# Kernel tuning notes

Hardware: AMD Instinct MI355X
Metric: run time of the kernel (lower is better)

The kernel has to match this reference:

```python
import jax, jax.numpy as jnp
import numpy as np

B, S, E, H = 2, 2048, 1024, 16
D = E // H  # head_dim = 64
NEG = -1e9


def setup_inputs() -> dict:
    key = jax.random.key(0)
    ks = jax.random.split(key, 12)
    def xavier(k, shape):
        fan_in, fan_out = shape[1], shape[0]
        lim = jnp.sqrt(6.0 / (fan_in + fan_out))
        return jax.random.uniform(k, shape, jnp.float32, -lim, lim)
    inp = {
        'Q_input': jax.random.normal(ks[0], (B, S, E), jnp.float32),
        'K_input': jax.random.normal(ks[1], (B, S, E), jnp.float32),
        'V_input': jax.random.normal(ks[2], (B, S, E), jnp.float32),
        'causal_mask': jnp.where(jnp.tril(jnp.ones((S, S), bool)), 0.0, NEG).astype(jnp.float32),
        'padding_mask': jnp.zeros((B, S), bool),
        'W_q': xavier(ks[3], (E, E)), 'b_q': jnp.zeros((E,), jnp.float32),
        'W_k': xavier(ks[4], (E, E)), 'b_k': jnp.zeros((E,), jnp.float32),
        'W_v': xavier(ks[5], (E, E)), 'b_v': jnp.zeros((E,), jnp.float32),
        'W_o': xavier(ks[6], (E, E)), 'b_o': jnp.zeros((E,), jnp.float32),
    }
    return inp


def reference(Q_input, K_input, V_input, causal_mask, padding_mask,
              W_q, b_q, W_k, b_k, W_v, b_v, W_o, b_o):
    b = Q_input.shape[0]
    # linear proj (torch convention: x @ W.T + b), split into heads -> [B,H,S,D]
    def proj(x, W, bias):
        y = x @ W.T + bias
        return y.reshape(b, -1, H, D).transpose(0, 2, 1, 3)
    Q = proj(Q_input, W_q, b_q)
    K = proj(K_input, W_k, b_k)
    V = proj(V_input, W_v, b_v)
    scale = 1.0 / jnp.sqrt(jnp.float32(D))
    scores = jnp.einsum('bhqd,bhkd->bhqk', Q, K) * scale  # [B,H,Sq,Sk]
    scores = jnp.where(padding_mask[:, None, None, :], NEG, scores)
    scores = scores + causal_mask  # broadcasts [Sq,Sk]
    attn = jax.nn.softmax(scores, axis=-1)
    ctx = jnp.einsum('bhqk,bhkd->bhqd', attn, V)
    ctx = ctx.transpose(0, 2, 1, 3).reshape(b, -1, E)
    return ctx @ W_o.T + b_o
```

## Files before the change

kernel.cpp:

```cpp
#include <hip/hip_runtime.h>
#include <hip/hip_bf16.h>

#define B_ 2
#define S_ 2048
#define E_ 1024
#define H_ 16
#define D_ 64

typedef __bf16 bf16x8 __attribute__((ext_vector_type(8)));
typedef __bf16 bf16x4 __attribute__((ext_vector_type(4)));
typedef float f32x4 __attribute__((ext_vector_type(4)));

#define MFMA16(a, b, c) __builtin_amdgcn_mfma_f32_16x16x32_bf16(a, b, c, 0, 0, 0)

__device__ __forceinline__ void cp16(const void* g, void* l) {
  __builtin_amdgcn_global_load_lds((const __attribute__((address_space(1))) void*)g,
                                   (__attribute__((address_space(3))) void*)l, 16, 0, 0);
}

__device__ __forceinline__ unsigned pack2(float a, float b) {
  unsigned short ua = __builtin_bit_cast(unsigned short, (__bf16)a);
  unsigned short ub = __builtin_bit_cast(unsigned short, (__bf16)b);
  return (unsigned)ua | ((unsigned)ub << 16);
}

__global__ __launch_bounds__(256) void cast_weights(
    const float* __restrict__ w0, const float* __restrict__ w1,
    const float* __restrict__ w2, const float* __restrict__ w3,
    __bf16* __restrict__ out)
{
  const float* srcs[4] = {w0, w1, w2, w3};
  const float* src = srcs[blockIdx.y];
  __bf16* dst = out + (size_t)blockIdx.y * E_ * E_;
  int i = (blockIdx.x * 256 + threadIdx.x) * 8;
  f32x4 a = *(const f32x4*)(src + i);
  f32x4 b = *(const f32x4*)(src + i + 4);
  bf16x8 o;
#pragma unroll
  for (int j = 0; j < 4; ++j) { o[j] = (__bf16)a[j]; o[j + 4] = (__bf16)b[j]; }
  *(bf16x8*)(dst + i) = o;
}

__global__ __launch_bounds__(256) void gemm_qkv(
    const float* __restrict__ Xq, const float* __restrict__ Xk,
    const float* __restrict__ Xv, const __bf16* __restrict__ Wc,
    const float* __restrict__ bq, const float* __restrict__ bk,
    const float* __restrict__ bv, __bf16* __restrict__ Proj)
{
  __shared__ __bf16 As[128 * 40];
  __shared__ __bf16 Bs[128 * 32];

  const int tid  = threadIdx.x;
  const int wave = tid >> 6, lane = tid & 63;
  const int l15  = lane & 15, quad = lane >> 4;
  const int wr = wave >> 1, wc = wave & 1;
  const int m0 = blockIdx.x * 128;
  const int wid = blockIdx.y >> 3;
  const int n0 = (blockIdx.y & 7) * 128;

  const float* X    = wid == 0 ? Xq : (wid == 1 ? Xk : Xv);
  const float* bias = wid == 0 ? bq : (wid == 1 ? bk : bv);
  const __bf16* W   = Wc + (size_t)wid * E_ * E_;
  __bf16* Out       = Proj + (size_t)wid * B_ * S_ * E_;

  f32x4 acc[4][4];
#pragma unroll
  for (int i = 0; i < 4; ++i)
#pragma unroll
    for (int j = 0; j < 4; ++j) acc[i][j] = (f32x4){0, 0, 0, 0};

  for (int k0 = 0; k0 < E_; k0 += 32) {
#pragma unroll
    for (int i = 0; i < 2; ++i) {
      int c = i * 256 + tid;
      int row = c >> 2, cg = c & 3;
      cp16(W + (size_t)(n0 + row) * E_ + k0 + cg * 8,
           (char*)Bs + i * 4096 + wave * 1024);
    }
#pragma unroll
    for (int i = 0; i < 2; ++i) {
      int c = i * 256 + tid;
      int row = c >> 2, cg = c & 3;
      f32x4 x0 = *(const f32x4*)(X + (size_t)(m0 + row) * E_ + k0 + cg * 8);
      f32x4 x1 = *(const f32x4*)(X + (size_t)(m0 + row) * E_ + k0 + cg * 8 + 4);
      bf16x8 v;
#pragma unroll
      for (int j = 0; j < 4; ++j) { v[j] = (__bf16)x0[j]; v[j + 4] = (__bf16)x1[j]; }
      *(bf16x8*)&As[row * 40 + cg * 8] = v;
    }
    __syncthreads();

    bf16x8 af[4], bfr[4];
#pragma unroll
    for (int ms = 0; ms < 4; ++ms) {
      int row = wr * 64 + ms * 16 + l15;
      af[ms] = *(const bf16x8*)&As[row * 40 + quad * 8];
    }
#pragma unroll
    for (int ns = 0; ns < 4; ++ns) {
      int row = wc * 64 + ns * 16 + l15;
      bfr[ns] = *(const bf16x8*)((const char*)Bs + row * 64 + quad * 16);
    }
#pragma unroll
    for (int ms = 0; ms < 4; ++ms)
#pragma unroll
      for (int ns = 0; ns < 4; ++ns)
        acc[ms][ns] = MFMA16(af[ms], bfr[ns], acc[ms][ns]);
    __syncthreads();
  }

#pragma unroll
  for (int ns = 0; ns < 4; ++ns) {
    int n = n0 + wc * 64 + ns * 16 + l15;
    float bv_ = bias[n];
#pragma unroll
    for (int ms = 0; ms < 4; ++ms)
#pragma unroll
      for (int r = 0; r < 4; ++r) {
        int m = m0 + wr * 64 + ms * 16 + quad * 4 + r;
        Out[(size_t)m * E_ + n] = (__bf16)(acc[ms][ns][r] + bv_);
      }
  }
}

__global__ __launch_bounds__(256) void gemm_out(
    const __bf16* __restrict__ X, const __bf16* __restrict__ W,
    const float* __restrict__ bias, float* __restrict__ out)
{
  __shared__ __bf16 As[64 * 32];
  __shared__ __bf16 Bs[128 * 32];

  const int tid  = threadIdx.x;
  const int wave = tid >> 6, lane = tid & 63;
  const int l15  = lane & 15, quad = lane >> 4;
  const int wr = wave >> 1, wc = wave & 1;
  const int m0 = blockIdx.x * 64;
  const int n0 = blockIdx.y * 128;

  f32x4 acc[2][4];
#pragma unroll
  for (int i = 0; i < 2; ++i)
#pragma unroll
    for (int j = 0; j < 4; ++j) acc[i][j] = (f32x4){0, 0, 0, 0};

  for (int k0 = 0; k0 < E_; k0 += 32) {
    {
      int row = tid >> 2, cg = tid & 3;
      cp16(X + (size_t)(m0 + row) * E_ + k0 + cg * 8,
           (char*)As + wave * 1024);
    }
#pragma unroll
    for (int i = 0; i < 2; ++i) {
      int c = i * 256 + tid;
      int row = c >> 2, cg = c & 3;
      cp16(W + (size_t)(n0 + row) * E_ + k0 + cg * 8,
           (char*)Bs + i * 4096 + wave * 1024);
    }
    __syncthreads();

    bf16x8 af[2], bfr[4];
#pragma unroll
    for (int ms = 0; ms < 2; ++ms) {
      int row = wr * 32 + ms * 16 + l15;
      af[ms] = *(const bf16x8*)((const char*)As + row * 64 + quad * 16);
    }
#pragma unroll
    for (int ns = 0; ns < 4; ++ns) {
      int row = wc * 64 + ns * 16 + l15;
      bfr[ns] = *(const bf16x8*)((const char*)Bs + row * 64 + quad * 16);
    }
#pragma unroll
    for (int ms = 0; ms < 2; ++ms)
#pragma unroll
      for (int ns = 0; ns < 4; ++ns)
        acc[ms][ns] = MFMA16(af[ms], bfr[ns], acc[ms][ns]);
    __syncthreads();
  }

#pragma unroll
  for (int ns = 0; ns < 4; ++ns) {
    int n = n0 + wc * 64 + ns * 16 + l15;
    float bv_ = bias[n];
#pragma unroll
    for (int ms = 0; ms < 2; ++ms)
#pragma unroll
      for (int r = 0; r < 4; ++r) {
        int m = m0 + wr * 32 + ms * 16 + quad * 4 + r;
        out[(size_t)m * E_ + n] = acc[ms][ns][r] + bv_;
      }
  }
}

__global__ __launch_bounds__(64) void transpose_v(
    const __bf16* __restrict__ Vp, __bf16* __restrict__ Vt)
{
  const int lane = threadIdx.x;
  const int b = blockIdx.y >> 4;
  const int h = blockIdx.y & 15;
  const int s0 = blockIdx.x * 64 + (lane & 7) * 8;
  const int d0 = (lane >> 3) * 8;

  bf16x8 in[8];
#pragma unroll
  for (int j = 0; j < 8; ++j)
    in[j] = *(const bf16x8*)&Vp[(((size_t)b * S_ + s0 + j) * H_ + h) * D_ + d0];
#pragma unroll
  for (int i = 0; i < 8; ++i) {
    bf16x8 t;
#pragma unroll
    for (int j = 0; j < 8; ++j) t[j] = in[j][i];
    *(bf16x8*)&Vt[(((size_t)b * H_ + h) * D_ + d0 + i) * S_ + s0] = t;
  }
}

__global__ __launch_bounds__(256) void attn_fwd(
    const __bf16* __restrict__ Qp, const __bf16* __restrict__ Kp,
    const __bf16* __restrict__ Vt, __bf16* __restrict__ Ctx)
{
  const int tid  = threadIdx.x;
  const int wave = tid >> 6;
  const int lane = tid & 63;
  const int l15  = lane & 15;
  const int quad = lane >> 4;
  const int t  = (int)gridDim.x - 1 - (int)blockIdx.x;
  const int q0 = t * 64;
  const int b  = blockIdx.y >> 4;
  const int h  = blockIdx.y & 15;
  const int wq0 = q0 + wave * 16;

  __shared__ __bf16 Ksh[2][64 * 64];
  __shared__ __bf16 Vsh[2][64 * 64];

  const __bf16* Khb = Kp + (size_t)b * S_ * E_ + h * 64;
  const __bf16* Vhb = Vt + ((size_t)b * H_ + h) * D_ * S_;

  bf16x8 qa[2];
#pragma unroll
  for (int kk = 0; kk < 2; ++kk) {
    bf16x8 q = *(const bf16x8*)&Qp[(size_t)(b * S_ + wq0 + l15) * E_ + h * 64 + kk * 32 + quad * 8];
#pragma unroll
    for (int j = 0; j < 8; ++j) q[j] = (__bf16)((float)q[j] * 0.125f);
    qa[kk] = q;
  }

  f32x4 o[4];
  float rs = 0.f;
#pragma unroll
  for (int ds = 0; ds < 4; ++ds) o[ds] = (f32x4){0, 0, 0, 0};

  const int nch = t + 1;

  auto stage = [&](int c, int bi) {
    const int kb0 = c * 64;
#pragma unroll
    for (int i = 0; i < 2; ++i) {
      int cc = i * 256 + tid;
      int key = cc >> 3, p = cc & 7;
      int pg = p ^ (key & 7);
      cp16(Khb + (size_t)(kb0 + key) * E_ + pg * 8,
           (char*)&Ksh[bi][0] + i * 4096 + wave * 1024);
    }
#pragma unroll
    for (int i = 0; i < 2; ++i) {
      int cc = i * 256 + tid;
      int d = cc >> 3, kp = cc & 7;
      int kpg = kp ^ (d & 7);
      cp16(Vhb + (size_t)d * S_ + kb0 + kpg * 8,
           (char*)&Vsh[bi][0] + i * 4096 + wave * 1024);
    }
  };

  stage(0, 0);

  const int hb = quad >> 1;
  const int s0l = (2 * (quad & 1)) * 16 + l15;
  const int s1l = s0l + 16;

  int cur = 0;
  for (int c = 0; c < nch; ++c) {
    if (c + 1 < nch) {
      stage(c + 1, cur ^ 1);
      asm volatile("s_waitcnt vmcnt(4)" ::: "memory");
    } else {
      asm volatile("s_waitcnt vmcnt(0)" ::: "memory");
    }
    __builtin_amdgcn_s_barrier();

    const int kb0 = c * 64;

    f32x4 sc[4];
    __builtin_amdgcn_s_setprio(1);
#pragma unroll
    for (int ks = 0; ks < 4; ++ks) {
      const char* Kpan = (const char*)&Ksh[cur][0];
      int row = ks * 16 + l15;
      bf16x8 kf0 = *(const bf16x8*)(Kpan + row * 128 + (((quad)     ^ (l15 & 7)) * 16));
      bf16x8 kf1 = *(const bf16x8*)(Kpan + row * 128 + (((4 + quad) ^ (l15 & 7)) * 16));
      f32x4 s = {0, 0, 0, 0};
      s = MFMA16(kf0, qa[0], s);
      s = MFMA16(kf1, qa[1], s);
      sc[ks] = s;
    }
    __builtin_amdgcn_s_setprio(0);

    unsigned pw[4][2];
    const bool msk = (kb0 + 63 > wq0);
    if (msk) {
#pragma unroll
      for (int ks = 0; ks < 4; ++ks) {
        float p[4];
#pragma unroll
        for (int r = 0; r < 4; ++r) {
          float e = __expf(sc[ks][r]);
          if (kb0 + ks * 16 + quad * 4 + r > wq0 + l15) e = 0.f;
          rs += e;
          p[r] = e;
        }
        pw[ks][0] = pack2(p[0], p[1]);
        pw[ks][1] = pack2(p[2], p[3]);
      }
    } else {
#pragma unroll
      for (int ks = 0; ks < 4; ++ks) {
        float p[4];
#pragma unroll
        for (int r = 0; r < 4; ++r) {
          float e = __expf(sc[ks][r]);
          rs += e;
          p[r] = e;
        }
        pw[ks][0] = pack2(p[0], p[1]);
        pw[ks][1] = pack2(p[2], p[3]);
      }
    }

    bf16x8 pf[2];
#pragma unroll
    for (int kk = 0; kk < 2; ++kk) {
      unsigned w[4];
#pragma unroll
      for (int wi = 0; wi < 4; ++wi) {
        int src = (wi & 2) ? s1l : s0l;
        unsigned g0 = __shfl(pw[2 * kk + 0][wi & 1], src, 64);
        unsigned g1 = __shfl(pw[2 * kk + 1][wi & 1], src, 64);
        w[wi] = hb ? g1 : g0;
      }
      union { unsigned u[4]; bf16x8 v; } cvt;
      cvt.u[0] = w[0]; cvt.u[1] = w[1]; cvt.u[2] = w[2]; cvt.u[3] = w[3];
      pf[kk] = cvt.v;
    }

    __builtin_amdgcn_s_setprio(1);
#pragma unroll
    for (int ds = 0; ds < 4; ++ds) {
      int row = ds * 16 + l15;
#pragma unroll
      for (int kk = 0; kk < 2; ++kk) {
        const char* Vpan = (const char*)&Vsh[cur][0];
        bf16x8 vf = *(const bf16x8*)(Vpan + row * 128 +
                                     (((kk * 4 + quad) ^ (l15 & 7)) * 16));
        o[ds] = MFMA16(pf[kk], vf, o[ds]);
      }
    }
    __builtin_amdgcn_s_setprio(0);

    asm volatile("" ::: "memory");
    __builtin_amdgcn_s_barrier();
    asm volatile("" ::: "memory");
    cur ^= 1;
  }

  float s = rs;
  s += __shfl_xor(s, 16, 64);
  s += __shfl_xor(s, 32, 64);
  float inv = 1.f / s;

#pragma unroll
  for (int r = 0; r < 4; ++r) {
    float invr = __shfl(inv, quad * 4 + r, 64);
    size_t base = (size_t)(b * S_ + wq0 + quad * 4 + r) * E_ + h * 64;
#pragma unroll
    for (int ds = 0; ds < 4; ++ds)
      Ctx[base + ds * 16 + l15] = (__bf16)(o[ds][r] * invr);
  }
}

extern "C" void kernel_launch(void* const* d_in, const int* in_sizes, int n_in,
                              void* d_out, int out_size, void* d_ws, size_t ws_size,
                              hipStream_t stream)
{
  const float* Qin = (const float*)d_in[0];
  const float* Kin = (const float*)d_in[1];
  const float* Vin = (const float*)d_in[2];
  const float* Wq = (const float*)d_in[5];
  const float* bq = (const float*)d_in[6];
  const float* Wk = (const float*)d_in[7];
  const float* bk = (const float*)d_in[8];
  const float* Wv = (const float*)d_in[9];
  const float* bv = (const float*)d_in[10];
  const float* Wo = (const float*)d_in[11];
  const float* bo = (const float*)d_in[12];

  __bf16* ws = (__bf16*)d_ws;
  const size_t WSZ = (size_t)E_ * E_;
  const size_t T   = (size_t)B_ * S_ * E_;
  __bf16* Wc   = ws;
  __bf16* Proj = ws + 4 * WSZ;
  __bf16* Vt   = ws + 4 * WSZ + 3 * T;
  __bf16* Ctx  = ws + 4 * WSZ + 4 * T;

  cast_weights<<<dim3(512, 4), 256, 0, stream>>>(Wq, Wk, Wv, Wo, Wc);
  gemm_qkv<<<dim3(32, 24), 256, 0, stream>>>(Qin, Kin, Vin, Wc, bq, bk, bv, Proj);
  transpose_v<<<dim3(S_ / 64, B_ * H_), 64, 0, stream>>>(Proj + 2 * T, Vt);
  attn_fwd<<<dim3(S_ / 64, B_ * H_), 256, 0, stream>>>(Proj, Proj + T, Vt, Ctx);
  gemm_out<<<dim3(64, 8), 256, 0, stream>>>(Ctx, Wc + 3 * WSZ, bo, (float*)d_out);
}
```

Before: 270.5 us.

## Pre-cast activations to bf16, use async LDS loads in QKV GEMM, widen attention tiles

The QKV GEMM's per-tile fp32-to-bf16 conversion is replaced by one cast kernel that converts weights and all three inputs to bf16 in workspace. The GEMM then loads the A tile with direct global-to-LDS copies, dropping the padded layout. The attention kernel now handles 128 query rows per block, each wave owning two 16-row fragments that share each staged K/V chunk. It also uses a diagonal block-to-tile mapping for causal load balance and sets occupancy via launch bounds. The trade-offs are an extra fp32-to-bf16 pass with more workspace traffic, more registers per wave in attention, and half as many attention blocks.

```diff
diff --git a/kernel.cpp b/kernel.cpp
--- a/kernel.cpp
+++ b/kernel.cpp
@@ -24,15 +24,21 @@
   return (unsigned)ua | ((unsigned)ub << 16);
 }
 
-__global__ __launch_bounds__(256) void cast_weights(
+__global__ __launch_bounds__(256) void cast_all(
     const float* __restrict__ w0, const float* __restrict__ w1,
     const float* __restrict__ w2, const float* __restrict__ w3,
-    __bf16* __restrict__ out)
-{
-  const float* srcs[4] = {w0, w1, w2, w3};
-  const float* src = srcs[blockIdx.y];
-  __bf16* dst = out + (size_t)blockIdx.y * E_ * E_;
-  int i = (blockIdx.x * 256 + threadIdx.x) * 8;
+    const float* __restrict__ x0, const float* __restrict__ x1,
+    const float* __restrict__ x2,
+    __bf16* __restrict__ dW, __bf16* __restrict__ dX)
+{
+  const float* srcs[7] = {w0, w1, w2, w3, x0, x1, x2};
+  const int y = blockIdx.y;
+  const bool isW = y < 4;
+  const size_t n = isW ? (size_t)E_ * E_ : (size_t)B_ * S_ * E_;
+  size_t i = ((size_t)blockIdx.x * 256 + threadIdx.x) * 8;
+  if (i >= n) return;
+  const float* src = srcs[y];
+  __bf16* dst = isW ? dW + (size_t)y * E_ * E_ : dX + (size_t)(y - 4) * B_ * S_ * E_;
   f32x4 a = *(const f32x4*)(src + i);
   f32x4 b = *(const f32x4*)(src + i + 4);
   bf16x8 o;
@@ -42,12 +48,11 @@
 }
 
 __global__ __launch_bounds__(256) void gemm_qkv(
-    const float* __restrict__ Xq, const float* __restrict__ Xk,
-    const float* __restrict__ Xv, const __bf16* __restrict__ Wc,
+    const __bf16* __restrict__ Xb, const __bf16* __restrict__ Wc,
     const float* __restrict__ bq, const float* __restrict__ bk,
     const float* __restrict__ bv, __bf16* __restrict__ Proj)
 {
-  __shared__ __bf16 As[128 * 40];
+  __shared__ __bf16 As[128 * 32];
   __shared__ __bf16 Bs[128 * 32];
 
   const int tid  = threadIdx.x;
@@ -58,7 +63,7 @@
   const int wid = blockIdx.y >> 3;
   const int n0 = (blockIdx.y & 7) * 128;
 
-  const float* X    = wid == 0 ? Xq : (wid == 1 ? Xk : Xv);
+  const __bf16* X   = Xb + (size_t)wid * B_ * S_ * E_;
   const float* bias = wid == 0 ? bq : (wid == 1 ? bk : bv);
   const __bf16* W   = Wc + (size_t)wid * E_ * E_;
   __bf16* Out       = Proj + (size_t)wid * B_ * S_ * E_;
@@ -70,6 +75,13 @@
     for (int j = 0; j < 4; ++j) acc[i][j] = (f32x4){0, 0, 0, 0};
 
   for (int k0 = 0; k0 < E_; k0 += 32) {
+#pragma unroll
+    for (int i = 0; i < 2; ++i) {
+      int c = i * 256 + tid;
+      int row = c >> 2, cg = c & 3;
+      cp16(X + (size_t)(m0 + row) * E_ + k0 + cg * 8,
+           (char*)As + i * 4096 + wave * 1024);
+    }
 #pragma unroll
     for (int i = 0; i < 2; ++i) {
       int c = i * 256 + tid;
@@ -77,24 +89,13 @@
       cp16(W + (size_t)(n0 + row) * E_ + k0 + cg * 8,
            (char*)Bs + i * 4096 + wave * 1024);
     }
-#pragma unroll
-    for (int i = 0; i < 2; ++i) {
-      int c = i * 256 + tid;
-      int row = c >> 2, cg = c & 3;
-      f32x4 x0 = *(const f32x4*)(X + (size_t)(m0 + row) * E_ + k0 + cg * 8);
-      f32x4 x1 = *(const f32x4*)(X + (size_t)(m0 + row) * E_ + k0 + cg * 8 + 4);
-      bf16x8 v;
-#pragma unroll
-      for (int j = 0; j < 4; ++j) { v[j] = (__bf16)x0[j]; v[j + 4] = (__bf16)x1[j]; }
-      *(bf16x8*)&As[row * 40 + cg * 8] = v;
-    }
     __syncthreads();
 
     bf16x8 af[4], bfr[4];
 #pragma unroll
     for (int ms = 0; ms < 4; ++ms) {
       int row = wr * 64 + ms * 16 + l15;
-      af[ms] = *(const bf16x8*)&As[row * 40 + quad * 8];
+      af[ms] = *(const bf16x8*)((const char*)As + row * 64 + quad * 16);
     }
 #pragma unroll
     for (int ns = 0; ns < 4; ++ns) {
@@ -213,7 +214,7 @@
   }
 }
 
-__global__ __launch_bounds__(256) void attn_fwd(
+__global__ __launch_bounds__(256, 4) void attn_fwd(
     const __bf16* __restrict__ Qp, const __bf16* __restrict__ Kp,
     const __bf16* __restrict__ Vt, __bf16* __restrict__ Ctx)
 {
@@ -222,11 +223,13 @@
   const int lane = tid & 63;
   const int l15  = lane & 15;
   const int quad = lane >> 4;
-  const int t  = (int)gridDim.x - 1 - (int)blockIdx.x;
-  const int q0 = t * 64;
-  const int b  = blockIdx.y >> 4;
-  const int h  = blockIdx.y & 15;
-  const int wq0 = q0 + wave * 16;
+  const int x = blockIdx.x;
+  const int y = blockIdx.y;
+  const int t = (x + y + ((y >> 4) << 2)) & 15;
+  const int q0 = t * 128;
+  const int b  = y >> 4;
+  const int h  = y & 15;
+  const int wq0 = q0 + wave * 32;
 
   __shared__ __bf16 Ksh[2][64 * 64];
   __shared__ __bf16 Vsh[2][64 * 64];
@@ -234,21 +237,26 @@
   const __bf16* Khb = Kp + (size_t)b * S_ * E_ + h * 64;
   const __bf16* Vhb = Vt + ((size_t)b * H_ + h) * D_ * S_;
 
-  bf16x8 qa[2];
-#pragma unroll
-  for (int kk = 0; kk < 2; ++kk) {
-    bf16x8 q = *(const bf16x8*)&Qp[(size_t)(b * S_ + wq0 + l15) * E_ + h * 64 + kk * 32 + quad * 8];
-#pragma unroll
-    for (int j = 0; j < 8; ++j) q[j] = (__bf16)((float)q[j] * 0.125f);
-    qa[kk] = q;
-  }
-
-  f32x4 o[4];
-  float rs = 0.f;
-#pragma unroll
-  for (int ds = 0; ds < 4; ++ds) o[ds] = (f32x4){0, 0, 0, 0};
-
-  const int nch = t + 1;
+  bf16x8 qa[2][2];
+#pragma unroll
+  for (int f = 0; f < 2; ++f)
+#pragma unroll
+    for (int kk = 0; kk < 2; ++kk) {
+      bf16x8 q = *(const bf16x8*)&Qp[(size_t)(b * S_ + wq0 + f * 16 + l15) * E_ +
+                                     h * 64 + kk * 32 + quad * 8];
+#pragma unroll
+      for (int j = 0; j < 8; ++j) q[j] = (__bf16)((float)q[j] * 0.125f);
+      qa[f][kk] = q;
+    }
+
+  f32x4 o[2][4];
+  float rs[2] = {0.f, 0.f};
+#pragma unroll
+  for (int f = 0; f < 2; ++f)
+#pragma unroll
+    for (int ds = 0; ds < 4; ++ds) o[f][ds] = (f32x4){0, 0, 0, 0};
+
+  const int nch = 2 * t + 2;
 
   auto stage = [&](int c, int bi) {
     const int kb0 = c * 64;
@@ -287,82 +295,92 @@
     __builtin_amdgcn_s_barrier();
 
     const int kb0 = c * 64;
-
-    f32x4 sc[4];
-    __builtin_amdgcn_s_setprio(1);
-#pragma unroll
-    for (int ks = 0; ks < 4; ++ks) {
-      const char* Kpan = (const char*)&Ksh[cur][0];
-      int row = ks * 16 + l15;
-      bf16x8 kf0 = *(const bf16x8*)(Kpan + row * 128 + (((quad)     ^ (l15 & 7)) * 16));
-      bf16x8 kf1 = *(const bf16x8*)(Kpan + row * 128 + (((4 + quad) ^ (l15 & 7)) * 16));
-      f32x4 s = {0, 0, 0, 0};
-      s = MFMA16(kf0, qa[0], s);
-      s = MFMA16(kf1, qa[1], s);
-      sc[ks] = s;
-    }
-    __builtin_amdgcn_s_setprio(0);
-
-    unsigned pw[4][2];
-    const bool msk = (kb0 + 63 > wq0);
-    if (msk) {
-#pragma unroll
-      for (int ks = 0; ks < 4; ++ks) {
-        float p[4];
-#pragma unroll
-        for (int r = 0; r < 4; ++r) {
-          float e = __expf(sc[ks][r]);
-          if (kb0 + ks * 16 + quad * 4 + r > wq0 + l15) e = 0.f;
-          rs += e;
-          p[r] = e;
+    const bool act0 = (kb0 <= wq0 + 15);
+    if (kb0 <= wq0 + 31) {
+      bf16x8 pfB[2][2];
+
+#pragma unroll
+      for (int f = 0; f < 2; ++f) {
+        const int wqf = wq0 + f * 16;
+        if (kb0 > wqf + 15) continue;
+
+        f32x4 sc[4];
+        __builtin_amdgcn_s_setprio(1);
+#pragma unroll
+        for (int ks = 0; ks < 4; ++ks) {
+          const char* Kpan = (const char*)&Ksh[cur][0];
+          int row = ks * 16 + l15;
+          bf16x8 kf0 = *(const bf16x8*)(Kpan + row * 128 + (((quad)     ^ (l15 & 7)) * 16));
+          bf16x8 kf1 = *(const bf16x8*)(Kpan + row * 128 + (((4 + quad) ^ (l15 & 7)) * 16));
+          f32x4 s = {0, 0, 0, 0};
+          s = MFMA16(kf0, qa[f][0], s);
+          s = MFMA16(kf1, qa[f][1], s);
+          sc[ks] = s;
         }
-        pw[ks][0] = pack2(p[0], p[1]);
-        pw[ks][1] = pack2(p[2], p[3]);
+        __builtin_amdgcn_s_setprio(0);
+
+        unsigned pw[4][2];
+        const bool msk = (kb0 + 63 > wqf);
+        if (msk) {
+#pragma unroll
+          for (int ks = 0; ks < 4; ++ks) {
+            float p[4];
+#pragma unroll
+            for (int r = 0; r < 4; ++r) {
+              float e = __expf(sc[ks][r]);
+              if (kb0 + ks * 16 + quad * 4 + r > wqf + l15) e = 0.f;
+              rs[f] += e;
+              p[r] = e;
+            }
+            pw[ks][0] = pack2(p[0], p[1]);
+            pw[ks][1] = pack2(p[2], p[3]);
+          }
+        } else {
+#pragma unroll
+          for (int ks = 0; ks < 4; ++ks) {
+            float p[4];
+#pragma unroll
+            for (int r = 0; r < 4; ++r) {
+              float e = __expf(sc[ks][r]);
+              rs[f] += e;
+              p[r] = e;
+            }
+            pw[ks][0] = pack2(p[0], p[1]);
+            pw[ks][1] = pack2(p[2], p[3]);
+          }
+        }
+
+#pragma unroll
+        for (int kk = 0; kk < 2; ++kk) {
+          unsigned w[4];
+#pragma unroll
+          for (int wi = 0; wi < 4; ++wi) {
+            int src = (wi & 2) ? s1l : s0l;
+            unsigned g0 = __shfl(pw[2 * kk + 0][wi & 1], src, 64);
+            unsigned g1 = __shfl(pw[2 * kk + 1][wi & 1], src, 64);
+            w[wi] = hb ? g1 : g0;
+          }
+          union { unsigned u[4]; bf16x8 v; } cvt;
+          cvt.u[0] = w[0]; cvt.u[1] = w[1]; cvt.u[2] = w[2]; cvt.u[3] = w[3];
+          pfB[f][kk] = cvt.v;
+        }
       }
-    } else {
-#pragma unroll
-      for (int ks = 0; ks < 4; ++ks) {
-        float p[4];
-#pragma unroll
-        for (int r = 0; r < 4; ++r) {
-          float e = __expf(sc[ks][r]);
-          rs += e;
-          p[r] = e;
+
+      __builtin_amdgcn_s_setprio(1);
+#pragma unroll
+      for (int ds = 0; ds < 4; ++ds) {
+        int row = ds * 16 + l15;
+#pragma unroll
+        for (int kk = 0; kk < 2; ++kk) {
+          const char* Vpan = (const char*)&Vsh[cur][0];
+          bf16x8 vf = *(const bf16x8*)(Vpan + row * 128 +
+                                       (((kk * 4 + quad) ^ (l15 & 7)) * 16));
+          if (act0) o[0][ds] = MFMA16(pfB[0][kk], vf, o[0][ds]);
+          o[1][ds] = MFMA16(pfB[1][kk], vf, o[1][ds]);
         }
-        pw[ks][0] = pack2(p[0], p[1]);
-        pw[ks][1] = pack2(p[2], p[3]);
       }
-    }
-
-    bf16x8 pf[2];
-#pragma unroll
-    for (int kk = 0; kk < 2; ++kk) {
-      unsigned w[4];
-#pragma unroll
-      for (int wi = 0; wi < 4; ++wi) {
-        int src = (wi & 2) ? s1l : s0l;
-        unsigned g0 = __shfl(pw[2 * kk + 0][wi & 1], src, 64);
-        unsigned g1 = __shfl(pw[2 * kk + 1][wi & 1], src, 64);
-        w[wi] = hb ? g1 : g0;
-      }
-      union { unsigned u[4]; bf16x8 v; } cvt;
-      cvt.u[0] = w[0]; cvt.u[1] = w[1]; cvt.u[2] = w[2]; cvt.u[3] = w[3];
-      pf[kk] = cvt.v;
-    }
-
-    __builtin_amdgcn_s_setprio(1);
-#pragma unroll
-    for (int ds = 0; ds < 4; ++ds) {
-      int row = ds * 16 + l15;
-#pragma unroll
-      for (int kk = 0; kk < 2; ++kk) {
-        const char* Vpan = (const char*)&Vsh[cur][0];
-        bf16x8 vf = *(const bf16x8*)(Vpan + row * 128 +
-                                     (((kk * 4 + quad) ^ (l15 & 7)) * 16));
-        o[ds] = MFMA16(pf[kk], vf, o[ds]);
-      }
-    }
-    __builtin_amdgcn_s_setprio(0);
+      __builtin_amdgcn_s_setprio(0);
+    }
 
     asm volatile("" ::: "memory");
     __builtin_amdgcn_s_barrier();
@@ -370,18 +388,21 @@
     cur ^= 1;
   }
 
-  float s = rs;
-  s += __shfl_xor(s, 16, 64);
-  s += __shfl_xor(s, 32, 64);
-  float inv = 1.f / s;
-
-#pragma unroll
-  for (int r = 0; r < 4; ++r) {
-    float invr = __shfl(inv, quad * 4 + r, 64);
-    size_t base = (size_t)(b * S_ + wq0 + quad * 4 + r) * E_ + h * 64;
-#pragma unroll
-    for (int ds = 0; ds < 4; ++ds)
-      Ctx[base + ds * 16 + l15] = (__bf16)(o[ds][r] * invr);
+#pragma unroll
+  for (int f = 0; f < 2; ++f) {
+    float s = rs[f];
+    s += __shfl_xor(s, 16, 64);
+    s += __shfl_xor(s, 32, 64);
+    float inv = 1.f / s;
+
+#pragma unroll
+    for (int r = 0; r < 4; ++r) {
+      float invr = __shfl(inv, quad * 4 + r, 64);
+      size_t base = (size_t)(b * S_ + wq0 + f * 16 + quad * 4 + r) * E_ + h * 64;
+#pragma unroll
+      for (int ds = 0; ds < 4; ++ds)
+        Ctx[base + ds * 16 + l15] = (__bf16)(o[f][ds][r] * invr);
+    }
   }
 }
 
@@ -408,10 +429,11 @@
   __bf16* Proj = ws + 4 * WSZ;
   __bf16* Vt   = ws + 4 * WSZ + 3 * T;
   __bf16* Ctx  = ws + 4 * WSZ + 4 * T;
-
-  cast_weights<<<dim3(512, 4), 256, 0, stream>>>(Wq, Wk, Wv, Wo, Wc);
-  gemm_qkv<<<dim3(32, 24), 256, 0, stream>>>(Qin, Kin, Vin, Wc, bq, bk, bv, Proj);
+  __bf16* Xbf  = ws + 4 * WSZ + 5 * T;
+
+  cast_all<<<dim3(2048, 7), 256, 0, stream>>>(Wq, Wk, Wv, Wo, Qin, Kin, Vin, Wc, Xbf);
+  gemm_qkv<<<dim3(32, 24), 256, 0, stream>>>(Xbf, Wc, bq, bk, bv, Proj);
   transpose_v<<<dim3(S_ / 64, B_ * H_), 64, 0, stream>>>(Proj + 2 * T, Vt);
-  attn_fwd<<<dim3(S_ / 64, B_ * H_), 256, 0, stream>>>(Proj, Proj + T, Vt, Ctx);
+  attn_fwd<<<dim3(S_ / 128, B_ * H_), 256, 0, stream>>>(Proj, Proj + T, Vt, Ctx);
   gemm_out<<<dim3(64, 8), 256, 0, stream>>>(Ctx, Wc + 3 * WSZ, bo, (float*)d_out);
 }
```

Result: faster. 252.4 us (-6.7%).

## Pre-cast inputs to bf16, double-buffer GEMMs, pair causal attention tiles, use exp2

Applied to the files above, without the earlier changes.

Activations are now cast to bf16 in a separate pass, which lets the QKV GEMM load them with async global-to-LDS copies. Both GEMMs switch to double-buffered LDS with waitcnt-based prefetch and raised MFMA priority. Attention blocks each handle two query tiles (t and 31-t) to even out causal work, and apply the softmax scale as log2(e)/8 so they can use exp2f. The extra cast pass writes and then rereads a full bf16 copy of the inputs, and halving the attention grid lowers the number of concurrent blocks.

```diff
diff --git a/kernel.cpp b/kernel.cpp
--- a/kernel.cpp
+++ b/kernel.cpp
@@ -24,15 +24,21 @@
   return (unsigned)ua | ((unsigned)ub << 16);
 }
 
-__global__ __launch_bounds__(256) void cast_weights(
+__global__ __launch_bounds__(256) void cast_all(
     const float* __restrict__ w0, const float* __restrict__ w1,
     const float* __restrict__ w2, const float* __restrict__ w3,
-    __bf16* __restrict__ out)
-{
-  const float* srcs[4] = {w0, w1, w2, w3};
-  const float* src = srcs[blockIdx.y];
-  __bf16* dst = out + (size_t)blockIdx.y * E_ * E_;
-  int i = (blockIdx.x * 256 + threadIdx.x) * 8;
+    const float* __restrict__ x0, const float* __restrict__ x1,
+    const float* __restrict__ x2,
+    __bf16* __restrict__ dW, __bf16* __restrict__ dX)
+{
+  const float* srcs[7] = {w0, w1, w2, w3, x0, x1, x2};
+  const int y = blockIdx.y;
+  const bool isW = y < 4;
+  const size_t n = isW ? (size_t)E_ * E_ : (size_t)B_ * S_ * E_;
+  size_t i = ((size_t)blockIdx.x * 256 + threadIdx.x) * 8;
+  if (i >= n) return;
+  const float* src = srcs[y];
+  __bf16* dst = isW ? dW + (size_t)y * E_ * E_ : dX + (size_t)(y - 4) * B_ * S_ * E_;
   f32x4 a = *(const f32x4*)(src + i);
   f32x4 b = *(const f32x4*)(src + i + 4);
   bf16x8 o;
@@ -42,13 +48,12 @@
 }
 
 __global__ __launch_bounds__(256) void gemm_qkv(
-    const float* __restrict__ Xq, const float* __restrict__ Xk,
-    const float* __restrict__ Xv, const __bf16* __restrict__ Wc,
+    const __bf16* __restrict__ Xb, const __bf16* __restrict__ Wc,
     const float* __restrict__ bq, const float* __restrict__ bk,
     const float* __restrict__ bv, __bf16* __restrict__ Proj)
 {
-  __shared__ __bf16 As[128 * 40];
-  __shared__ __bf16 Bs[128 * 32];
+  __shared__ __bf16 As[2][128 * 32];
+  __shared__ __bf16 Bs[2][128 * 32];
 
   const int tid  = threadIdx.x;
   const int wave = tid >> 6, lane = tid & 63;
@@ -58,55 +63,68 @@
   const int wid = blockIdx.y >> 3;
   const int n0 = (blockIdx.y & 7) * 128;
 
-  const float* X    = wid == 0 ? Xq : (wid == 1 ? Xk : Xv);
+  const __bf16* X   = Xb + (size_t)wid * B_ * S_ * E_;
   const float* bias = wid == 0 ? bq : (wid == 1 ? bk : bv);
   const __bf16* W   = Wc + (size_t)wid * E_ * E_;
   __bf16* Out       = Proj + (size_t)wid * B_ * S_ * E_;
 
-  f32x4 acc[4][4];
-#pragma unroll
-  for (int i = 0; i < 4; ++i)
-#pragma unroll
-    for (int j = 0; j < 4; ++j) acc[i][j] = (f32x4){0, 0, 0, 0};
-
-  for (int k0 = 0; k0 < E_; k0 += 32) {
+  auto stage = [&](int k0, int bi) {
+#pragma unroll
+    for (int i = 0; i < 2; ++i) {
+      int c = i * 256 + tid;
+      int row = c >> 2, cg = c & 3;
+      cp16(X + (size_t)(m0 + row) * E_ + k0 + cg * 8,
+           (char*)&As[bi][0] + i * 4096 + wave * 1024);
+    }
 #pragma unroll
     for (int i = 0; i < 2; ++i) {
       int c = i * 256 + tid;
       int row = c >> 2, cg = c & 3;
       cp16(W + (size_t)(n0 + row) * E_ + k0 + cg * 8,
-           (char*)Bs + i * 4096 + wave * 1024);
-    }
-#pragma unroll
-    for (int i = 0; i < 2; ++i) {
-      int c = i * 256 + tid;
-      int row = c >> 2, cg = c & 3;
-      f32x4 x0 = *(const f32x4*)(X + (size_t)(m0 + row) * E_ + k0 + cg * 8);
-      f32x4 x1 = *(const f32x4*)(X + (size_t)(m0 + row) * E_ + k0 + cg * 8 + 4);
-      bf16x8 v;
-#pragma unroll
-      for (int j = 0; j < 4; ++j) { v[j] = (__bf16)x0[j]; v[j + 4] = (__bf16)x1[j]; }
-      *(bf16x8*)&As[row * 40 + cg * 8] = v;
-    }
-    __syncthreads();
+           (char*)&Bs[bi][0] + i * 4096 + wave * 1024);
+    }
+  };
+
+  f32x4 acc[4][4];
+#pragma unroll
+  for (int i = 0; i < 4; ++i)
+#pragma unroll
+    for (int j = 0; j < 4; ++j) acc[i][j] = (f32x4){0, 0, 0, 0};
+
+  stage(0, 0);
+  int cur = 0;
+  for (int k0 = 0; k0 < E_; k0 += 32) {
+    if (k0 + 32 < E_) {
+      stage(k0 + 32, cur ^ 1);
+      asm volatile("s_waitcnt vmcnt(4)" ::: "memory");
+    } else {
+      asm volatile("s_waitcnt vmcnt(0)" ::: "memory");
+    }
+    __builtin_amdgcn_s_barrier();
 
     bf16x8 af[4], bfr[4];
 #pragma unroll
     for (int ms = 0; ms < 4; ++ms) {
       int row = wr * 64 + ms * 16 + l15;
-      af[ms] = *(const bf16x8*)&As[row * 40 + quad * 8];
+      af[ms] = *(const bf16x8*)((const char*)&As[cur][0] + row * 64 + quad * 16);
     }
 #pragma unroll
     for (int ns = 0; ns < 4; ++ns) {
       int row = wc * 64 + ns * 16 + l15;
-      bfr[ns] = *(const bf16x8*)((const char*)Bs + row * 64 + quad * 16);
-    }
+      bfr[ns] = *(const bf16x8*)((const char*)&Bs[cur][0] + row * 64 + quad * 16);
+    }
+    __builtin_amdgcn_s_setprio(1);
 #pragma unroll
     for (int ms = 0; ms < 4; ++ms)
 #pragma unroll
       for (int ns = 0; ns < 4; ++ns)
         acc[ms][ns] = MFMA16(af[ms], bfr[ns], acc[ms][ns]);
-    __syncthreads();
+    __builtin_amdgcn_s_setprio(0);
+
+    asm volatile("" ::: "memory");
+    __builtin_amdgcn_s_barrier();
+    asm volatile("" ::: "memory");
+    cur ^= 1;
   }
 
 #pragma unroll
@@ -127,8 +145,8 @@
     const __bf16* __restrict__ X, const __bf16* __restrict__ W,
     const float* __restrict__ bias, float* __restrict__ out)
 {
-  __shared__ __bf16 As[64 * 32];
-  __shared__ __bf16 Bs[128 * 32];
+  __shared__ __bf16 As[2][64 * 32];
+  __shared__ __bf16 Bs[2][128 * 32];
 
   const int tid  = threadIdx.x;
   const int wave = tid >> 6, lane = tid & 63;
@@ -137,44 +155,61 @@
   const int m0 = blockIdx.x * 64;
   const int n0 = blockIdx.y * 128;
 
-  f32x4 acc[2][4];
-#pragma unroll
-  for (int i = 0; i < 2; ++i)
-#pragma unroll
-    for (int j = 0; j < 4; ++j) acc[i][j] = (f32x4){0, 0, 0, 0};
-
-  for (int k0 = 0; k0 < E_; k0 += 32) {
+  auto stage = [&](int k0, int bi) {
     {
       int row = tid >> 2, cg = tid & 3;
       cp16(X + (size_t)(m0 + row) * E_ + k0 + cg * 8,
-           (char*)As + wave * 1024);
+           (char*)&As[bi][0] + wave * 1024);
     }
 #pragma unroll
     for (int i = 0; i < 2; ++i) {
       int c = i * 256 + tid;
       int row = c >> 2, cg = c & 3;
       cp16(W + (size_t)(n0 + row) * E_ + k0 + cg * 8,
-           (char*)Bs + i * 4096 + wave * 1024);
-    }
-    __syncthreads();
+           (char*)&Bs[bi][0] + i * 4096 + wave * 1024);
+    }
+  };
+
+  f32x4 acc[2][4];
+#pragma unroll
+  for (int i = 0; i < 2; ++i)
+#pragma unroll
+    for (int j = 0; j < 4; ++j) acc[i][j] = (f32x4){0, 0, 0, 0};
+
+  stage(0, 0);
+  int cur = 0;
+  for (int k0 = 0; k0 < E_; k0 += 32) {
+    if (k0 + 32 < E_) {
+      stage(k0 + 32, cur ^ 1);
+      asm volatile("s_waitcnt vmcnt(3)" ::: "memory");
+    } else {
+      asm volatile("s_waitcnt vmcnt(0)" ::: "memory");
+    }
+    __builtin_amdgcn_s_barrier();
 
     bf16x8 af[2], bfr[4];
 #pragma unroll
     for (int ms = 0; ms < 2; ++ms) {
       int row = wr * 32 + ms * 16 + l15;
-      af[ms] = *(const bf16x8*)((const char*)As + row * 64 + quad * 16);
+      af[ms] = *(const bf16x8*)((const char*)&As[cur][0] + row * 64 + quad * 16);
     }
 #pragma unroll
     for (int ns = 0; ns < 4; ++ns) {
       int row = wc * 64 + ns * 16 + l15;
-      bfr[ns] = *(const bf16x8*)((const char*)Bs + row * 64 + quad * 16);
-    }
+      bfr[ns] = *(const bf16x8*)((const char*)&Bs[cur][0] + row * 64 + quad * 16);
+    }
+    __builtin_amdgcn_s_setprio(1);
 #pragma unroll
     for (int ms = 0; ms < 2; ++ms)
 #pragma unroll
       for (int ns = 0; ns < 4; ++ns)
         acc[ms][ns] = MFMA16(af[ms], bfr[ns], acc[ms][ns]);
-    __syncthreads();
+    __builtin_amdgcn_s_setprio(0);
+
+    asm volatile("" ::: "memory");
+    __builtin_amdgcn_s_barrier();
+    asm volatile("" ::: "memory");
+    cur ^= 1;
   }
 
 #pragma unroll
@@ -213,7 +248,7 @@
   }
 }
 
-__global__ __launch_bounds__(256) void attn_fwd(
+__global__ __launch_bounds__(256, 4) void attn_fwd(
     const __bf16* __restrict__ Qp, const __bf16* __restrict__ Kp,
     const __bf16* __restrict__ Vt, __bf16* __restrict__ Ctx)
 {
@@ -222,33 +257,16 @@
   const int lane = tid & 63;
   const int l15  = lane & 15;
   const int quad = lane >> 4;
-  const int t  = (int)gridDim.x - 1 - (int)blockIdx.x;
-  const int q0 = t * 64;
-  const int b  = blockIdx.y >> 4;
-  const int h  = blockIdx.y & 15;
-  const int wq0 = q0 + wave * 16;
+  const int x = blockIdx.x;
+  const int y = blockIdx.y;
+  const int b = y >> 4;
+  const int h = y & 15;
 
   __shared__ __bf16 Ksh[2][64 * 64];
   __shared__ __bf16 Vsh[2][64 * 64];
 
   const __bf16* Khb = Kp + (size_t)b * S_ * E_ + h * 64;
   const __bf16* Vhb = Vt + ((size_t)b * H_ + h) * D_ * S_;
-
-  bf16x8 qa[2];
-#pragma unroll
-  for (int kk = 0; kk < 2; ++kk) {
-    bf16x8 q = *(const bf16x8*)&Qp[(size_t)(b * S_ + wq0 + l15) * E_ + h * 64 + kk * 32 + quad * 8];
-#pragma unroll
-    for (int j = 0; j < 8; ++j) q[j] = (__bf16)((float)q[j] * 0.125f);
-    qa[kk] = q;
-  }
-
-  f32x4 o[4];
-  float rs = 0.f;
-#pragma unroll
-  for (int ds = 0; ds < 4; ++ds) o[ds] = (f32x4){0, 0, 0, 0};
-
-  const int nch = t + 1;
 
   auto stage = [&](int c, int bi) {
     const int kb0 = c * 64;
@@ -270,118 +288,141 @@
     }
   };
 
-  stage(0, 0);
-
   const int hb = quad >> 1;
   const int s0l = (2 * (quad & 1)) * 16 + l15;
   const int s1l = s0l + 16;
-
-  int cur = 0;
-  for (int c = 0; c < nch; ++c) {
-    if (c + 1 < nch) {
-      stage(c + 1, cur ^ 1);
-      asm volatile("s_waitcnt vmcnt(4)" ::: "memory");
-    } else {
-      asm volatile("s_waitcnt vmcnt(0)" ::: "memory");
-    }
-    __builtin_amdgcn_s_barrier();
-
-    const int kb0 = c * 64;
-
-    f32x4 sc[4];
-    __builtin_amdgcn_s_setprio(1);
-#pragma unroll
-    for (int ks = 0; ks < 4; ++ks) {
-      const char* Kpan = (const char*)&Ksh[cur][0];
-      int row = ks * 16 + l15;
-      bf16x8 kf0 = *(const bf16x8*)(Kpan + row * 128 + (((quad)     ^ (l15 & 7)) * 16));
-      bf16x8 kf1 = *(const bf16x8*)(Kpan + row * 128 + (((4 + quad) ^ (l15 & 7)) * 16));
-      f32x4 s = {0, 0, 0, 0};
-      s = MFMA16(kf0, qa[0], s);
-      s = MFMA16(kf1, qa[1], s);
-      sc[ks] = s;
-    }
-    __builtin_amdgcn_s_setprio(0);
-
-    unsigned pw[4][2];
-    const bool msk = (kb0 + 63 > wq0);
-    if (msk) {
+  const float esc = 0.18033688011f;
+
+  for (int ti = 0; ti < 2; ++ti) {
+    const int t = ti ? 31 - x : x;
+    const int q0 = t * 64;
+    const int wq0 = q0 + wave * 16;
+
+    bf16x8 qa[2];
+#pragma unroll
+    for (int kk = 0; kk < 2; ++kk) {
+      bf16x8 q = *(const bf16x8*)&Qp[(size_t)(b * S_ + wq0 + l15) * E_ +
+                                     h * 64 + kk * 32 + quad * 8];
+#pragma unroll
+      for (int j = 0; j < 8; ++j) q[j] = (__bf16)((float)q[j] * esc);
+      qa[kk] = q;
+    }
+
+    f32x4 o[4];
+    float rs = 0.f;
+#pragma unroll
+    for (int ds = 0; ds < 4; ++ds) o[ds] = (f32x4){0, 0, 0, 0};
+
+    const int nch = t + 1;
+
+    stage(0, 0);
+    int cur = 0;
+    for (int c = 0; c < nch; ++c) {
+      if (c + 1 < nch) {
+        stage(c + 1, cur ^ 1);
+        asm volatile("s_waitcnt vmcnt(4)" ::: "memory");
+      } else {
+        asm volatile("s_waitcnt vmcnt(0)" ::: "memory");
+      }
+      __builtin_amdgcn_s_barrier();
+
+      const int kb0 = c * 64;
+
+      f32x4 sc[4];
+      __builtin_amdgcn_s_setprio(1);
 #pragma unroll
       for (int ks = 0; ks < 4; ++ks) {
-        float p[4];
-#pragma unroll
-        for (int r = 0; r < 4; ++r) {
-          float e = __expf(sc[ks][r]);
-          if (kb0 + ks * 16 + quad * 4 + r > wq0 + l15) e = 0.f;
-          rs += e;
-          p[r] = e;
+        const char* Kpan = (const char*)&Ksh[cur][0];
+        int row = ks * 16 + l15;
+        bf16x8 kf0 = *(const bf16x8*)(Kpan + row * 128 + (((quad)     ^ (l15 & 7)) * 16));
+        bf16x8 kf1 = *(const bf16x8*)(Kpan + row * 128 + (((4 + quad) ^ (l15 & 7)) * 16));
+        f32x4 s = {0, 0, 0, 0};
+        s = MFMA16(kf0, qa[0], s);
+        s = MFMA16(kf1, qa[1], s);
+        sc[ks] = s;
+      }
+      __builtin_amdgcn_s_setprio(0);
+
+      unsigned pw[4][2];
+      const bool msk = (kb0 + 63 > wq0);
+      if (msk) {
+#pragma unroll
+        for (int ks = 0; ks < 4; ++ks) {
+          float p[4];
+#pragma unroll
+          for (int r = 0; r < 4; ++r) {
+            float e = exp2f(sc[ks][r]);
+            if (kb0 + ks * 16 + quad * 4 + r > wq0 + l15) e = 0.f;
+            rs += e;
+            p[r] = e;
+          }
+          pw[ks][0] = pack2(p[0], p[1]);
+          pw[ks][1] = pack2(p[2], p[3]);
         }
-        pw[ks][0] = pack2(p[0], p[1]);
-        pw[ks][1] = pack2(p[2], p[3]);
-      }
-    } else {
-#pragma unroll
-      for (int ks = 0; ks < 4; ++ks) {
-        float p[4];
-#pragma unroll
-        for (int r = 0; r < 4; ++r) {
-          float e = __expf(sc[ks][r]);
-          rs += e;
-          p[r] = e;
+      } else {
+#pragma unroll
+        for (int ks = 0; ks < 4; ++ks) {
+          float p[4];
+#pragma unroll
+          for (int r = 0; r < 4; ++r) {
+            float e = exp2f(sc[ks][r]);
+            rs += e;
+            p[r] = e;
+          }
+          pw[ks][0] = pack2(p[0], p[1]);
+          pw[ks][1] = pack2(p[2], p[3]);
         }
-        pw[ks][0] = pack2(p[0], p[1]);
-        pw[ks][1] = pack2(p[2], p[3]);
-      }
-    }
-
-    bf16x8 pf[2];
-#pragma unroll
-    for (int kk = 0; kk < 2; ++kk) {
-      unsigned w[4];
-#pragma unroll
-      for (int wi = 0; wi < 4; ++wi) {
-        int src = (wi & 2) ? s1l : s0l;
-        unsigned g0 = __shfl(pw[2 * kk + 0][wi & 1], src, 64);
-        unsigned g1 = __shfl(pw[2 * kk + 1][wi & 1], src, 64);
-        w[wi] = hb ? g1 : g0;
-      }
-      union { unsigned u[4]; bf16x8 v; } cvt;
-      cvt.u[0] = w[0]; cvt.u[1] = w[1]; cvt.u[2] = w[2]; cvt.u[3] = w[3];
-      pf[kk] = cvt.v;
-    }
-
-    __builtin_amdgcn_s_setprio(1);
-#pragma unroll
-    for (int ds = 0; ds < 4; ++ds) {
-      int row = ds * 16 + l15;
+      }
+
+      bf16x8 pf[2];
 #pragma unroll
       for (int kk = 0; kk < 2; ++kk) {
-        const char* Vpan = (const char*)&Vsh[cur][0];
-        bf16x8 vf = *(const bf16x8*)(Vpan + row * 128 +
-                                     (((kk * 4 + quad) ^ (l15 & 7)) * 16));
-        o[ds] = MFMA16(pf[kk], vf, o[ds]);
-      }
-    }
-    __builtin_amdgcn_s_setprio(0);
-
-    asm volatile("" ::: "memory");
-    __builtin_amdgcn_s_barrier();
-    asm volatile("" ::: "memory");
-    cur ^= 1;
-  }
-
-  float s = rs;
-  s += __shfl_xor(s, 16, 64);
-  s += __shfl_xor(s, 32, 64);
-  float inv = 1.f / s;
-
-#pragma unroll
-  for (int r = 0; r < 4; ++r) {
-    float invr = __shfl(inv, quad * 4 + r, 64);
-    size_t base = (size_t)(b * S_ + wq0 + quad * 4 + r) * E_ + h * 64;
-#pragma unroll
-    for (int ds = 0; ds < 4; ++ds)
-      Ctx[base + ds * 16 + l15] = (__bf16)(o[ds][r] * invr);
+        unsigned w[4];
+#pragma unroll
+        for (int wi = 0; wi < 4; ++wi) {
+          int src = (wi & 2) ? s1l : s0l;
+          unsigned g0 = __shfl(pw[2 * kk + 0][wi & 1], src, 64);
+          unsigned g1 = __shfl(pw[2 * kk + 1][wi & 1], src, 64);
+          w[wi] = hb ? g1 : g0;
+        }
+        union { unsigned u[4]; bf16x8 v; } cvt;
+        cvt.u[0] = w[0]; cvt.u[1] = w[1]; cvt.u[2] = w[2]; cvt.u[3] = w[3];
+        pf[kk] = cvt.v;
+      }
+
+      __builtin_amdgcn_s_setprio(1);
+#pragma unroll
+      for (int ds = 0; ds < 4; ++ds) {
+        int row = ds * 16 + l15;
+#pragma unroll
+        for (int kk = 0; kk < 2; ++kk) {
+          const char* Vpan = (const char*)&Vsh[cur][0];
+          bf16x8 vf = *(const bf16x8*)(Vpan + row * 128 +
+                                       (((kk * 4 + quad) ^ (l15 & 7)) * 16));
+          o[ds] = MFMA16(pf[kk], vf, o[ds]);
+        }
+      }
+      __builtin_amdgcn_s_setprio(0);
+
+      asm volatile("" ::: "memory");
+      __builtin_amdgcn_s_barrier();
+      asm volatile("" ::: "memory");
+      cur ^= 1;
+    }
+
+    float s = rs;
+    s += __shfl_xor(s, 16, 64);
+    s += __shfl_xor(s, 32, 64);
+    float inv = 1.f / s;
+
+#pragma unroll
+    for (int r = 0; r < 4; ++r) {
+      float invr = __shfl(inv, quad * 4 + r, 64);
+      size_t base = (size_t)(b * S_ + wq0 + quad * 4 + r) * E_ + h * 64;
+#pragma unroll
+      for (int ds = 0; ds < 4; ++ds)
+        Ctx[base + ds * 16 + l15] = (__bf16)(o[ds][r] * invr);
+    }
   }
 }
 
@@ -408,10 +449,11 @@
   __bf16* Proj = ws + 4 * WSZ;
   __bf16* Vt   = ws + 4 * WSZ + 3 * T;
   __bf16* Ctx  = ws + 4 * WSZ + 4 * T;
-
-  cast_weights<<<dim3(512, 4), 256, 0, stream>>>(Wq, Wk, Wv, Wo, Wc);
-  gemm_qkv<<<dim3(32, 24), 256, 0, stream>>>(Qin, Kin, Vin, Wc, bq, bk, bv, Proj);
+  __bf16* Xbf  = ws + 4 * WSZ + 5 * T;
+
+  cast_all<<<dim3(2048, 7), 256, 0, stream>>>(Wq, Wk, Wv, Wo, Qin, Kin, Vin, Wc, Xbf);
+  gemm_qkv<<<dim3(32, 24), 256, 0, stream>>>(Xbf, Wc, bq, bk, bv, Proj);
   transpose_v<<<dim3(S_ / 64, B_ * H_), 64, 0, stream>>>(Proj + 2 * T, Vt);
-  attn_fwd<<<dim3(S_ / 64, B_ * H_), 256, 0, stream>>>(Proj, Proj + T, Vt, Ctx);
+  attn_fwd<<<dim3(16, B_ * H_), 256, 0, stream>>>(Proj, Proj + T, Vt, Ctx);
   gemm_out<<<dim3(64, 8), 256, 0, stream>>>(Ctx, Wc + 3 * WSZ, bo, (float*)d_out);
 }
```

Result: faster. 244.2 us (-9.7%).
